# Kernel optimization log

Measured on AMD Instinct MI355X. Metric: run time of the kernel, lower is better.

Reference implementation:

```python
import jax, jax.numpy as jnp
import numpy as np

B, T, D = 2, 2048, 2048
H = 8
KEY_DIM, VAL_DIM = 1024, 2048   # expand_k=0.5, expand_v=1.0
HK, HV = KEY_DIM // H, VAL_DIM // H
LOW_RANK = 16
GATE_NORM = 16.0
CHUNK = 64
HIDDEN = (D * 4 * 2 // 3 + 63) // 64 * 64  # 5504, exactly as GLUFFN.__init__
EPS = 1e-6


def rmsnorm(x, w):
    return x * jax.lax.rsqrt(jnp.mean(x * x, axis=-1, keepdims=True) + EPS) * w


def setup_inputs() -> dict:
    key = jax.random.key(0)
    ks = jax.random.split(key, 12)
    w = lambda k, s: jax.random.normal(k, s, jnp.float32) * 0.02
    return {
        "x": jax.random.normal(ks[0], (B, T, D), jnp.float32),
        "norm1_w": jnp.ones((D,), jnp.float32),
        "wq": w(ks[1], (D, KEY_DIM)),
        "wk": w(ks[2], (D, KEY_DIM)),
        "wv": w(ks[3], (D, VAL_DIM)),
        "gk_w1": w(ks[4], (D, LOW_RANK)),
        "gk_w2": w(ks[5], (LOW_RANK, KEY_DIM)),
        "gk_b": jnp.zeros((KEY_DIM,), jnp.float32),
        "wg": w(ks[6], (D, VAL_DIM)),
        "gnorm_w": jnp.ones((HV,), jnp.float32),
        "wo": w(ks[7], (VAL_DIM, D)),
        "ffn_norm_w": jnp.ones((D,), jnp.float32),
        "w_gate": w(ks[8], (D, HIDDEN)),
        "w_up": w(ks[9], (D, HIDDEN)),
        "w_down": w(ks[10], (HIDDEN, D)),
    }


def _gla(h, wq, wk, wv, gk_w1, gk_w2, gk_b, wg, gnorm_w, wo):
    # Gated linear attention, chunk-parallel form (fla-style):
    #   S_t = diag(exp(g_t)) S_{t-1} + k_t^T v_t ;  o_t = q_t S_t
    Bb, Tt, _ = h.shape
    nc = Tt // CHUNK

    def split(t, hd):  # [B,T,H*hd] -> [nc,B,H,CHUNK,hd]
        t = t.reshape(Bb, nc, CHUNK, H, hd)
        return jnp.transpose(t, (1, 0, 3, 2, 4))

    q = split(h @ wq, HK) * (HK ** -0.5)
    k = split(h @ wk, HK)
    v = split(h @ wv, HV)
    # low-rank forget gate, log-sigmoid scaled by gate_logit_normalizer=16
    g = split(jax.nn.log_sigmoid(h @ gk_w1 @ gk_w2 + gk_b) / GATE_NORM, HK)

    mask = jnp.tril(jnp.ones((CHUNK, CHUNK), jnp.float32))

    def step(S, inp):
        qc, kc, vc, gc = inp                       # [B,H,C,*]
        b = jnp.cumsum(gc, axis=-2)                # cumulative log-decay within chunk
        qe = qc * jnp.exp(b)
        A = jnp.einsum('bhik,bhjk->bhij', qe, kc * jnp.exp(-b)) * mask
        o = jnp.einsum('bhck,bhkv->bhcv', qe, S) + jnp.einsum('bhij,bhjv->bhiv', A, vc)
        bl = b[:, :, -1:, :]                       # decay to end of chunk
        S = jnp.exp(bl[:, :, 0, :])[..., None] * S + \
            jnp.einsum('bhck,bhcv->bhkv', kc * jnp.exp(bl - b), vc)
        return S, o

    S0 = jnp.zeros((Bb, H, HK, HV), h.dtype)
    _, o = jax.lax.scan(step, S0, (q, k, v, g))    # o: [nc,B,H,C,HV]
    o = jnp.transpose(o, (1, 0, 3, 2, 4)).reshape(Bb, Tt, H, HV)

    gate = (h @ wg).reshape(Bb, Tt, H, HV)
    # per-head RMSNorm + swish output gate (FusedRMSNormSwishGate)
    o = rmsnorm(o, gnorm_w) * gate * jax.nn.sigmoid(gate)
    return o.reshape(Bb, Tt, VAL_DIM) @ wo


def reference(x, norm1_w, wq, wk, wv, gk_w1, gk_w2, gk_b, wg, gnorm_w, wo,
              ffn_norm_w, w_gate, w_up, w_down):
    h = rmsnorm(x, norm1_w)
    x = x + _gla(h, wq, wk, wv, gk_w1, gk_w2, gk_b, wg, gnorm_w, wo)
    h2 = rmsnorm(x, ffn_norm_w)
    ffn = (jax.nn.silu(h2 @ w_gate) * (h2 @ w_up)) @ w_down  # GLUFFN, dropout=eval
    return x + ffn
```

## Files before the change

kernel.cpp:

```cpp
#include <hip/hip_runtime.h>

typedef unsigned short u16;
typedef __attribute__((ext_vector_type(8))) short bh8;
typedef __attribute__((ext_vector_type(4))) float f4;

__device__ __forceinline__ float bf2f(u16 u) {
  union { unsigned int i; float f; } x; x.i = ((unsigned int)u) << 16; return x.f;
}
__device__ __forceinline__ u16 f2bf(float f) {
  union { float f; unsigned int i; } x; x.f = f;
  unsigned int r = x.i + 0x7fffu + ((x.i >> 16) & 1u);
  return (u16)(r >> 16);
}
__device__ __forceinline__ f4 mfma16(bh8 a, bh8 b, f4 c) {
  return __builtin_amdgcn_mfma_f32_16x16x32_bf16(a, b, c, 0, 0, 0);
}
__device__ __forceinline__ void gload16(const void* g, void* l) {
  __builtin_amdgcn_global_load_lds(
      (const __attribute__((address_space(1))) void*)g,
      (__attribute__((address_space(3))) void*)l, 16, 0, 0);
}
__device__ __forceinline__ void store_out(float* p, float v) { *p = v; }
__device__ __forceinline__ void store_out(u16* p, float v) { *p = f2bf(v); }

__device__ __forceinline__ bh8 rd8(const u16* arr, int row, int col, int rowbytes) {
  return *(const bh8*)((const char*)arr + row * rowbytes + ((col * 2) ^ ((row & 7) << 4)));
}

__global__ __launch_bounds__(256)
void wtrans_k(const float* __restrict__ src, u16* __restrict__ dst, int R, int C) {
  __shared__ float tile[32][33];
  int tx = threadIdx.x & 31, ty = threadIdx.x >> 5;
  int c0 = blockIdx.x * 32, r0 = blockIdx.y * 32;
#pragma unroll
  for (int yy = 0; yy < 32; yy += 8)
    tile[ty + yy][tx] = src[(size_t)(r0 + ty + yy) * C + c0 + tx];
  __syncthreads();
#pragma unroll
  for (int yy = 0; yy < 32; yy += 8)
    dst[(size_t)(c0 + ty + yy) * R + r0 + tx] = f2bf(tile[tx][ty + yy]);
}

__global__ __launch_bounds__(256)
void rmsnorm_k(const float* __restrict__ x, const float* __restrict__ w,
               u16* __restrict__ out) {
  int row = blockIdx.x, t = threadIdx.x;
  const float* xr = x + (size_t)row * 2048;
  float4 a = ((const float4*)xr)[t * 2];
  float4 b = ((const float4*)xr)[t * 2 + 1];
  float ss = a.x*a.x + a.y*a.y + a.z*a.z + a.w*a.w
           + b.x*b.x + b.y*b.y + b.z*b.z + b.w*b.w;
#pragma unroll
  for (int s = 32; s > 0; s >>= 1) ss += __shfl_xor(ss, s, 64);
  __shared__ float red[4];
  if ((t & 63) == 0) red[t >> 6] = ss;
  __syncthreads();
  float rr = rsqrtf((red[0] + red[1] + red[2] + red[3]) * (1.0f / 2048.0f) + 1e-6f);
  float v[8] = {a.x, a.y, a.z, a.w, b.x, b.y, b.z, b.w};
  int c0 = t * 8;
  u16* orow = out + (size_t)row * 2048 + c0;
#pragma unroll
  for (int j = 0; j < 8; ++j) orow[j] = f2bf(v[j] * rr * w[c0 + j]);
}

template <int EPI, typename OutT>
__global__ __launch_bounds__(256)
void gemm_bt(const u16* __restrict__ A, const u16* __restrict__ Bt,
             OutT* C, const void* aux, float scale, int M, int N, int K) {
  __shared__ u16 As[4096];
  __shared__ u16 Bs[4096];
  int t = threadIdx.x, lane = t & 63, wave = t >> 6;
  int m0 = blockIdx.y * 128, n0 = blockIdx.x * 128;
  int wr = (wave >> 1) * 64, wc = (wave & 1) * 64;
  int c_ = lane & 15, r_ = lane >> 4;
  f4 z4 = {0.f, 0.f, 0.f, 0.f};
  f4 acc[4][4];
#pragma unroll
  for (int m = 0; m < 4; ++m)
#pragma unroll
    for (int n = 0; n < 4; ++n) acc[m][n] = z4;

  const u16* Ab = A + (size_t)m0 * K;
  const u16* Bb = Bt + (size_t)n0 * K;
  int srow = t >> 2, scol = (t & 3) * 8;
  char* AsB = (char*)As;
  char* BsB = (char*)Bs;
  int ldsbase = wave * 1024;

  for (int k0 = 0; k0 < K; k0 += 32) {
#pragma unroll
    for (int p = 0; p < 2; ++p) {
      gload16(Ab + (size_t)(p * 64 + srow) * K + k0 + scol, AsB + p * 4096 + ldsbase);
      gload16(Bb + (size_t)(p * 64 + srow) * K + k0 + scol, BsB + p * 4096 + ldsbase);
    }
    __syncthreads();
    bh8 af[4], bfr[4];
#pragma unroll
    for (int m = 0; m < 4; ++m) af[m] = *(const bh8*)&As[(wr + m * 16 + c_) * 32 + r_ * 8];
#pragma unroll
    for (int n = 0; n < 4; ++n) bfr[n] = *(const bh8*)&Bs[(wc + n * 16 + c_) * 32 + r_ * 8];
#pragma unroll
    for (int m = 0; m < 4; ++m)
#pragma unroll
      for (int n = 0; n < 4; ++n) acc[m][n] = mfma16(af[m], bfr[n], acc[m][n]);
    __syncthreads();
  }
#pragma unroll
  for (int m = 0; m < 4; ++m) {
#pragma unroll
    for (int r = 0; r < 4; ++r) {
      int rowg = m0 + wr + m * 16 + r_ * 4 + r;
      size_t rb = (size_t)rowg * N;
#pragma unroll
      for (int n = 0; n < 4; ++n) {
        int colg = n0 + wc + n * 16 + c_;
        float val = acc[m][n][r];
        if (EPI == 0) {
          store_out(&C[rb + colg], val * scale);
        } else if (EPI == 1) {
          store_out(&C[rb + colg], val + ((const float*)aux)[rb + colg]);
        } else if (EPI == 2) {
          float gv = bf2f(((const u16*)aux)[rb + colg]);
          store_out(&C[rb + colg], val * (gv / (1.f + expf(-gv))));
        } else {
          int bb = rowg >> 11, t2 = rowg & 2047;
          int pan = ((bb << 5) + (t2 >> 6)) * 8 + (colg >> 8);
          int ii = t2 & 63, vv = colg & 255;
          *(u16*)((char*)C + (size_t)pan * 32768 + vv * 128 + ((ii * 2) ^ ((vv & 7) << 4)))
              = f2bf(val);
        }
      }
    }
  }
}

__global__ __launch_bounds__(256)
void lowrank_k(const u16* __restrict__ h, const float* __restrict__ w1,
               const float* __restrict__ w2, const float* __restrict__ bias,
               float* __restrict__ g) {
  int row = blockIdx.x, t = threadIdx.x, lane = t & 63, wave = t >> 6;
  const u16* hr = h + (size_t)row * 2048;
  bh8 hv = *(const bh8*)&hr[t * 8];
  float p[16];
#pragma unroll
  for (int j = 0; j < 16; ++j) p[j] = 0.f;
#pragma unroll
  for (int kk = 0; kk < 8; ++kk) {
    float f = bf2f((u16)hv[kk]);
    const float* wrow = w1 + (size_t)(t * 8 + kk) * 16;
#pragma unroll
    for (int j = 0; j < 16; ++j) p[j] += f * wrow[j];
  }
#pragma unroll
  for (int j = 0; j < 16; ++j)
#pragma unroll
    for (int s = 32; s > 0; s >>= 1) p[j] += __shfl_xor(p[j], s, 64);
  __shared__ float gl[4][16];
  if (lane == 0) {
#pragma unroll
    for (int j = 0; j < 16; ++j) gl[wave][j] = p[j];
  }
  __syncthreads();
  float glow[16];
#pragma unroll
  for (int j = 0; j < 16; ++j) glow[j] = gl[0][j] + gl[1][j] + gl[2][j] + gl[3][j];
  float* grow = g + (size_t)row * 1024;
#pragma unroll
  for (int nn = 0; nn < 4; ++nn) {
    int n = nn * 256 + t;
    float z = bias[n];
#pragma unroll
    for (int j = 0; j < 16; ++j) z += glow[j] * w2[j * 1024 + n];
    float ls = fminf(z, 0.f) - log1pf(expf(-fabsf(z)));
    grow[n] = ls * (1.0f / 16.0f);
  }
}

__global__ __launch_bounds__(128)
void gprep_k(u16* __restrict__ q, u16* __restrict__ k, const float* __restrict__ g,
             u16* __restrict__ keT, float* __restrict__ ebl) {
  int bid = blockIdx.x;
  int h = bid & 7, bc = bid >> 3;
  int b = bc >> 5, c = bc & 31;
  int ch = threadIdx.x;
  size_t base = ((size_t)(b * 2048 + c * 64)) * 1024 + h * 128 + ch;
  char* keTp = (char*)keT + (size_t)bid * 16384 + ch * 128;
  int sw = (ch & 7) << 4;
  float bacc = 0.f;
  for (int i8 = 0; i8 < 8; ++i8) {
    u16 kp[8];
#pragma unroll
    for (int e = 0; e < 8; ++e) {
      size_t off = base + (size_t)(i8 * 8 + e) * 1024;
      bacc += g[off];
      float eb = __expf(bacc);
      float reb = __builtin_amdgcn_rcpf(eb);
      float qv = bf2f(q[off]), kv = bf2f(k[off]);
      q[off] = f2bf(qv * eb);
      u16 kev = f2bf(kv * reb);
      k[off] = kev;
      kp[e] = kev;
    }
    *(bh8*)(keTp + ((i8 * 16) ^ sw)) = *(const bh8*)kp;
  }
  ebl[(size_t)bid * 128 + ch] = __expf(bacc);
}

__global__ __launch_bounds__(256)
void gla_scan(const u16* __restrict__ qg, const u16* __restrict__ kg,
              const u16* __restrict__ keTg, const u16* __restrict__ vTg,
              const float* __restrict__ eblg, float* __restrict__ outp) {
  __shared__ u16 qeL[64 * 128];
  __shared__ u16 keL[64 * 128];
  __shared__ u16 kTL[128 * 64];
  __shared__ u16 vTL[64 * 64];
  __shared__ u16 AL[64 * 64];
  __shared__ u16 SbL[64 * 128];
  __shared__ float SfL[64][133];

  int t = threadIdx.x, lane = t & 63, w = t >> 6;
  int vb = blockIdx.x & 3, bh = blockIdx.x >> 2;
  int b = bh >> 3, h = bh & 7;
  int c_ = lane & 15, r_ = lane >> 4;
  f4 z4 = {0.f, 0.f, 0.f, 0.f};

  for (int i = t; i < 64 * 128; i += 256) SbL[i] = 0;
  for (int i = t; i < 64 * 133; i += 256) ((float*)SfL)[i] = 0.f;

  const char* qbase = (const char*)qg + (size_t)b * 2048 * 2048 + h * 256;
  const char* kbase = (const char*)kg + (size_t)b * 2048 * 2048 + h * 256;
  int rowoff = (t >> 4) * 2048 + (t & 15) * 16;
  int4 pq[4], pk[4], pkt[4], pvt[2];

#define LOADCH(cc)                                                              \
  {                                                                             \
    const char* qc = qbase + (size_t)(cc) * 64 * 2048;                          \
    const char* kc = kbase + (size_t)(cc) * 64 * 2048;                          \
    int panel_ = ((b * 32 + (cc)) * 8 + h);                                     \
    const char* ktc = (const char*)keTg + (size_t)panel_ * 16384;               \
    const char* vtc = (const char*)vTg + (size_t)panel_ * 32768 + vb * 8192;    \
    _Pragma("unroll")                                                           \
    for (int j = 0; j < 4; ++j) {                                               \
      pq[j] = *(const int4*)(qc + j * 16 * 2048 + rowoff);                      \
      pk[j] = *(const int4*)(kc + j * 16 * 2048 + rowoff);                      \
      pkt[j] = *(const int4*)(ktc + j * 4096 + t * 16);                         \
    }                                                                           \
    _Pragma("unroll")                                                           \
    for (int j = 0; j < 2; ++j) pvt[j] = *(const int4*)(vtc + j * 4096 + t * 16); \
  }

  LOADCH(0);
  for (int c = 0; c < 32; ++c) {
#pragma unroll
    for (int j = 0; j < 4; ++j) {
      int L = j * 4096 + t * 16;
      int d = (L & ~255) | ((L & 255) ^ (((L >> 8) & 7) << 4));
      *(int4*)((char*)qeL + d) = pq[j];
      *(int4*)((char*)keL + d) = pk[j];
      *(int4*)((char*)kTL + L) = pkt[j];
    }
#pragma unroll
    for (int j = 0; j < 2; ++j) *(int4*)((char*)vTL + j * 4096 + t * 16) = pvt[j];
    if (c < 31) LOADCH(c + 1);
    int panel = ((b * 32 + c) * 8 + h);
    float eblr[2][4];
#pragma unroll
    for (int kt = 0; kt < 2; ++kt)
#pragma unroll
      for (int r = 0; r < 4; ++r)
        eblr[kt][r] = eblg[(size_t)panel * 128 + w * 32 + kt * 16 + r_ * 4 + r];
    __syncthreads();

    f4 accA[4] = {z4, z4, z4, z4};
    f4 accS[2][4] = {{z4, z4, z4, z4}, {z4, z4, z4, z4}};
#pragma unroll
    for (int ks = 0; ks < 4; ++ks) {
      bh8 a = rd8(qeL, w * 16 + c_, ks * 32 + r_ * 8, 256);
#pragma unroll
      for (int n = 0; n < 4; ++n)
        accA[n] = mfma16(a, rd8(keL, n * 16 + c_, ks * 32 + r_ * 8, 256), accA[n]);
    }
#pragma unroll
    for (int ks = 0; ks < 2; ++ks) {
      bh8 bf_[4];
#pragma unroll
      for (int n = 0; n < 4; ++n) bf_[n] = rd8(vTL, n * 16 + c_, ks * 32 + r_ * 8, 128);
#pragma unroll
      for (int kt = 0; kt < 2; ++kt) {
        bh8 a = rd8(kTL, w * 32 + kt * 16 + c_, ks * 32 + r_ * 8, 128);
#pragma unroll
        for (int n = 0; n < 4; ++n) accS[kt][n] = mfma16(a, bf_[n], accS[kt][n]);
      }
    }
#pragma unroll
    for (int n = 0; n < 4; ++n)
#pragma unroll
      for (int r = 0; r < 4; ++r) {
        int i = w * 16 + r_ * 4 + r, j = n * 16 + c_;
        *(u16*)((char*)AL + i * 128 + ((j * 2) ^ ((i & 7) << 4))) =
            (j <= i) ? f2bf(accA[n][r]) : (u16)0;
      }
    __syncthreads();

    f4 acco[4] = {z4, z4, z4, z4};
#pragma unroll
    for (int ks = 0; ks < 4; ++ks) {
      bh8 a = rd8(qeL, w * 16 + c_, ks * 32 + r_ * 8, 256);
#pragma unroll
      for (int n = 0; n < 4; ++n)
        acco[n] = mfma16(a, rd8(SbL, n * 16 + c_, ks * 32 + r_ * 8, 256), acco[n]);
    }
#pragma unroll
    for (int ks = 0; ks < 2; ++ks) {
      bh8 a = rd8(AL, w * 16 + c_, ks * 32 + r_ * 8, 128);
#pragma unroll
      for (int n = 0; n < 4; ++n)
        acco[n] = mfma16(a, rd8(vTL, n * 16 + c_, ks * 32 + r_ * 8, 128), acco[n]);
    }
    {
      size_t obase = (size_t)(b * 2048 + c * 64 + w * 16 + r_ * 4) * 2048 + h * 256 + vb * 64;
#pragma unroll
      for (int n = 0; n < 4; ++n)
#pragma unroll
        for (int r = 0; r < 4; ++r)
          outp[obase + (size_t)r * 2048 + n * 16 + c_] = acco[n][r];
    }
    __syncthreads();

#pragma unroll
    for (int kt = 0; kt < 2; ++kt)
#pragma unroll
      for (int n = 0; n < 4; ++n)
#pragma unroll
        for (int r = 0; r < 4; ++r) {
          int kk = w * 32 + kt * 16 + r_ * 4 + r;
          int vcol = n * 16 + c_;
          float nv = eblr[kt][r] * (SfL[vcol][kk] + accS[kt][n][r]);
          SfL[vcol][kk] = nv;
          *(u16*)((char*)SbL + vcol * 256 + ((kk * 2) ^ ((vcol & 7) << 4))) = f2bf(nv);
        }
    __syncthreads();
  }
#undef LOADCH
}

__global__ __launch_bounds__(256)
void ogate_k(const float* __restrict__ o, const u16* __restrict__ gate,
             const float* __restrict__ gw, u16* __restrict__ og) {
  int tok = blockIdx.x, t = threadIdx.x;
  int head = t >> 5, l32 = t & 31, v0 = l32 * 8;
  size_t base = (size_t)tok * 2048 + head * 256 + v0;
  float4 a = *(const float4*)&o[base];
  float4 b = *(const float4*)&o[base + 4];
  float ov[8] = {a.x, a.y, a.z, a.w, b.x, b.y, b.z, b.w};
  float ss = 0.f;
#pragma unroll
  for (int j = 0; j < 8; ++j) ss += ov[j] * ov[j];
#pragma unroll
  for (int s = 16; s > 0; s >>= 1) ss += __shfl_xor(ss, s, 32);
  float rr = rsqrtf(ss * (1.0f / 256.0f) + 1e-6f);
#pragma unroll
  for (int j = 0; j < 8; ++j) {
    float gv = bf2f(gate[base + j]);
    float val = ov[j] * rr * gw[v0 + j];
    og[base + j] = f2bf(val * gv / (1.f + expf(-gv)));
  }
}

extern "C" void kernel_launch(void* const* d_in, const int* in_sizes, int n_in,
                              void* d_out, int out_size, void* d_ws, size_t ws_size,
                              hipStream_t stream) {
  (void)in_sizes; (void)n_in; (void)out_size; (void)ws_size;
  const float* x = (const float*)d_in[0];
  const float* n1w = (const float*)d_in[1];
  const float* wq = (const float*)d_in[2];
  const float* wk = (const float*)d_in[3];
  const float* wv = (const float*)d_in[4];
  const float* gw1 = (const float*)d_in[5];
  const float* gw2 = (const float*)d_in[6];
  const float* gb = (const float*)d_in[7];
  const float* wg = (const float*)d_in[8];
  const float* gnw = (const float*)d_in[9];
  const float* wo = (const float*)d_in[10];
  const float* fnw = (const float*)d_in[11];
  const float* wgate = (const float*)d_in[12];
  const float* wup = (const float*)d_in[13];
  const float* wdown = (const float*)d_in[14];
  float* out = (float*)d_out;

  char* ws = (char*)d_ws;
  size_t off = 0;
  auto alloc = [&](size_t bytes) { size_t p = off; off += (bytes + 255) & ~(size_t)255; return p; };
  u16* wqT = (u16*)(ws + alloc(2ull * 1024 * 2048));
  u16* wkT = (u16*)(ws + alloc(2ull * 1024 * 2048));
  u16* wvT = (u16*)(ws + alloc(2ull * 2048 * 2048));
  u16* wgT = (u16*)(ws + alloc(2ull * 2048 * 2048));
  u16* woT = (u16*)(ws + alloc(2ull * 2048 * 2048));
  u16* wgateT = (u16*)(ws + alloc(2ull * 5504 * 2048));
  u16* wupT = (u16*)(ws + alloc(2ull * 5504 * 2048));
  u16* wdT = (u16*)(ws + alloc(2ull * 2048 * 5504));
  u16* h_bf = (u16*)(ws + alloc(2ull * 4096 * 2048));
  u16* q_bf = (u16*)(ws + alloc(2ull * 4096 * 1024));
  u16* k_bf = (u16*)(ws + alloc(2ull * 4096 * 1024));
  u16* vT_g = (u16*)(ws + alloc(2ull * 4096 * 2048));
  u16* gate_bf = (u16*)(ws + alloc(2ull * 4096 * 2048));
  float* g_f = (float*)(ws + alloc(4ull * 4096 * 1024));
  float* o_f = (float*)(ws + alloc(4ull * 4096 * 2048));
  u16* gH = (u16*)(ws + alloc(2ull * 4096 * 5504));
  float* ebl_g = (float*)(ws + alloc(4ull * 512 * 128));
  u16* keT_g = h_bf;
  u16* og = h_bf;
  u16* h2 = q_bf;
  float* x2 = o_f;
  u16* mid = gH;

  dim3 blk(256);
  wtrans_k<<<dim3(32, 64), blk, 0, stream>>>(wq, wqT, 2048, 1024);
  wtrans_k<<<dim3(32, 64), blk, 0, stream>>>(wk, wkT, 2048, 1024);
  wtrans_k<<<dim3(64, 64), blk, 0, stream>>>(wv, wvT, 2048, 2048);
  wtrans_k<<<dim3(64, 64), blk, 0, stream>>>(wg, wgT, 2048, 2048);
  wtrans_k<<<dim3(64, 64), blk, 0, stream>>>(wo, woT, 2048, 2048);
  wtrans_k<<<dim3(172, 64), blk, 0, stream>>>(wgate, wgateT, 2048, 5504);
  wtrans_k<<<dim3(172, 64), blk, 0, stream>>>(wup, wupT, 2048, 5504);
  wtrans_k<<<dim3(64, 172), blk, 0, stream>>>(wdown, wdT, 5504, 2048);

  rmsnorm_k<<<4096, blk, 0, stream>>>(x, n1w, h_bf);

  gemm_bt<0, u16><<<dim3(8, 32), blk, 0, stream>>>(h_bf, wqT, q_bf, nullptr, 0.08838834764831845f, 4096, 1024, 2048);
  gemm_bt<0, u16><<<dim3(8, 32), blk, 0, stream>>>(h_bf, wkT, k_bf, nullptr, 1.f, 4096, 1024, 2048);
  gemm_bt<3, u16><<<dim3(16, 32), blk, 0, stream>>>(h_bf, wvT, vT_g, nullptr, 1.f, 4096, 2048, 2048);
  gemm_bt<0, u16><<<dim3(16, 32), blk, 0, stream>>>(h_bf, wgT, gate_bf, nullptr, 1.f, 4096, 2048, 2048);
  lowrank_k<<<4096, blk, 0, stream>>>(h_bf, gw1, gw2, gb, g_f);

  gprep_k<<<512, dim3(128), 0, stream>>>(q_bf, k_bf, g_f, keT_g, ebl_g);

  gla_scan<<<64, blk, 0, stream>>>(q_bf, k_bf, keT_g, vT_g, ebl_g, o_f);

  ogate_k<<<4096, blk, 0, stream>>>(o_f, gate_bf, gnw, og);

  gemm_bt<1, float><<<dim3(16, 32), blk, 0, stream>>>(og, woT, x2, x, 1.f, 4096, 2048, 2048);

  rmsnorm_k<<<4096, blk, 0, stream>>>(x2, fnw, h2);

  gemm_bt<0, u16><<<dim3(43, 32), blk, 0, stream>>>(h2, wgateT, gH, nullptr, 1.f, 4096, 5504, 2048);
  gemm_bt<2, u16><<<dim3(43, 32), blk, 0, stream>>>(h2, wupT, mid, gH, 1.f, 4096, 5504, 2048);
  gemm_bt<1, float><<<dim3(16, 32), blk, 0, stream>>>(mid, wdT, out, x2, 1.f, 4096, 2048, 5504);
}
```

Baseline: 1.141 ms.

## Replace GEMM with triple-buffered 128x256 kernel and fuse projection GEMMs

Replaces the single-stage 128x128 GEMM with a 128x256-tile kernel. It triple-buffers LDS through direct global-to-LDS loads, uses an XOR-swizzled LDS layout, and splits each k-step into two MFMA phases separated by barriers, with s_setprio raised around the MFMAs. Block order is remapped in groups of eight to improve cache locality. The q/k and v/gate projections are each merged into one wider GEMM, relying on the transposed weights being adjacent in the workspace. The gate and up weights are row-interleaved so a single GEMM pairs each gate value with its up value through a lane shuffle and writes the SwiGLU result directly. This removes the separate gate-output round trip and several launches, but raises register and LDS pressure per block.

```diff
diff --git a/kernel.cpp b/kernel.cpp
--- a/kernel.cpp
+++ b/kernel.cpp
@@ -20,15 +20,14 @@
       (const __attribute__((address_space(1))) void*)g,
       (__attribute__((address_space(3))) void*)l, 16, 0, 0);
 }
-__device__ __forceinline__ void store_out(float* p, float v) { *p = v; }
-__device__ __forceinline__ void store_out(u16* p, float v) { *p = f2bf(v); }
 
 __device__ __forceinline__ bh8 rd8(const u16* arr, int row, int col, int rowbytes) {
   return *(const bh8*)((const char*)arr + row * rowbytes + ((col * 2) ^ ((row & 7) << 4)));
 }
 
 __global__ __launch_bounds__(256)
-void wtrans_k(const float* __restrict__ src, u16* __restrict__ dst, int R, int C) {
+void wtrans_k(const float* __restrict__ src, u16* __restrict__ dst, int R, int C,
+              int rmul, int roff) {
   __shared__ float tile[32][33];
   int tx = threadIdx.x & 31, ty = threadIdx.x >> 5;
   int c0 = blockIdx.x * 32, r0 = blockIdx.y * 32;
@@ -38,7 +37,7 @@
   __syncthreads();
 #pragma unroll
   for (int yy = 0; yy < 32; yy += 8)
-    dst[(size_t)(c0 + ty + yy) * R + r0 + tx] = f2bf(tile[tx][ty + yy]);
+    dst[(size_t)((c0 + ty + yy) * rmul + roff) * R + r0 + tx] = f2bf(tile[tx][ty + yy]);
 }
 
 __global__ __launch_bounds__(256)
@@ -64,70 +63,137 @@
 }
 
 template <int EPI, typename OutT>
-__global__ __launch_bounds__(256)
-void gemm_bt(const u16* __restrict__ A, const u16* __restrict__ Bt,
-             OutT* C, const void* aux, float scale, int M, int N, int K) {
-  __shared__ u16 As[4096];
-  __shared__ u16 Bs[4096];
-  int t = threadIdx.x, lane = t & 63, wave = t >> 6;
-  int m0 = blockIdx.y * 128, n0 = blockIdx.x * 128;
-  int wr = (wave >> 1) * 64, wc = (wave & 1) * 64;
+__global__ __launch_bounds__(256, 2)
+void gemm2(const u16* __restrict__ A, const u16* __restrict__ Bt,
+           OutT* __restrict__ C, void* __restrict__ aux, float scale,
+           int M, int N, int K, int gx) {
+  __shared__ char lds[73728];
+  int t = threadIdx.x, lane = t & 63, w = t >> 6;
   int c_ = lane & 15, r_ = lane >> 4;
+
+  int nwg = gridDim.x;
+  int wg = (blockIdx.x & 7) * (nwg >> 3) + (blockIdx.x >> 3);
+  int gy = nwg / gx;
+  int bx = wg / gy, by = wg % gy;
+  int m0 = by * 128, n0 = bx * 256;
+
+  const size_t ldA = K, ldB = K;
+
+  auto stageA = [&](int kt, int slot, int h) {
+    int p = h * 256 + t;
+    int cc = p ^ ((p >> 3) & 7);
+    int m = cc >> 2, kb = cc & 3;
+    const char* src = (const char*)A + ((size_t)(m0 + m) * ldA + kt * 32) * 2 + kb * 16;
+    char* dst = lds + slot * 24576 + h * 4096 + w * 1024;
+    gload16(src, dst);
+  };
+  auto stageB = [&](int kt, int slot, int qq, int j) {
+    int p = qq * 512 + j * 256 + t;
+    int cc = p ^ ((p >> 3) & 7);
+    int n = cc >> 2, kb = cc & 3;
+    const char* src = (const char*)Bt + ((size_t)(n0 + n) * ldB + kt * 32) * 2 + kb * 16;
+    char* dst = lds + slot * 24576 + 8192 + (qq * 8192 + j * 4096) + w * 1024;
+    gload16(src, dst);
+  };
+  auto rdA = [&](int slot, int mb) -> bh8 {
+    int cc = (mb * 16 + c_) * 4 + r_;
+    int p = cc ^ ((cc >> 3) & 7);
+    return *(const bh8*)(lds + slot * 24576 + p * 16);
+  };
+  auto rdB = [&](int slot, int nb) -> bh8 {
+    int cc = (w * 64 + nb * 16 + c_) * 4 + r_;
+    int p = cc ^ ((cc >> 3) & 7);
+    return *(const bh8*)(lds + slot * 24576 + 8192 + p * 16);
+  };
+
   f4 z4 = {0.f, 0.f, 0.f, 0.f};
-  f4 acc[4][4];
-#pragma unroll
-  for (int m = 0; m < 4; ++m)
-#pragma unroll
-    for (int n = 0; n < 4; ++n) acc[m][n] = z4;
-
-  const u16* Ab = A + (size_t)m0 * K;
-  const u16* Bb = Bt + (size_t)n0 * K;
-  int srow = t >> 2, scol = (t & 3) * 8;
-  char* AsB = (char*)As;
-  char* BsB = (char*)Bs;
-  int ldsbase = wave * 1024;
-
-  for (int k0 = 0; k0 < K; k0 += 32) {
-#pragma unroll
-    for (int p = 0; p < 2; ++p) {
-      gload16(Ab + (size_t)(p * 64 + srow) * K + k0 + scol, AsB + p * 4096 + ldsbase);
-      gload16(Bb + (size_t)(p * 64 + srow) * K + k0 + scol, BsB + p * 4096 + ldsbase);
-    }
-    __syncthreads();
-    bh8 af[4], bfr[4];
-#pragma unroll
-    for (int m = 0; m < 4; ++m) af[m] = *(const bh8*)&As[(wr + m * 16 + c_) * 32 + r_ * 8];
-#pragma unroll
-    for (int n = 0; n < 4; ++n) bfr[n] = *(const bh8*)&Bs[(wc + n * 16 + c_) * 32 + r_ * 8];
-#pragma unroll
-    for (int m = 0; m < 4; ++m)
-#pragma unroll
-      for (int n = 0; n < 4; ++n) acc[m][n] = mfma16(af[m], bfr[n], acc[m][n]);
-    __syncthreads();
-  }
-#pragma unroll
-  for (int m = 0; m < 4; ++m) {
-#pragma unroll
-    for (int r = 0; r < 4; ++r) {
-      int rowg = m0 + wr + m * 16 + r_ * 4 + r;
-      size_t rb = (size_t)rowg * N;
-#pragma unroll
-      for (int n = 0; n < 4; ++n) {
-        int colg = n0 + wc + n * 16 + c_;
-        float val = acc[m][n][r];
-        if (EPI == 0) {
-          store_out(&C[rb + colg], val * scale);
-        } else if (EPI == 1) {
-          store_out(&C[rb + colg], val + ((const float*)aux)[rb + colg]);
-        } else if (EPI == 2) {
-          float gv = bf2f(((const u16*)aux)[rb + colg]);
-          store_out(&C[rb + colg], val * (gv / (1.f + expf(-gv))));
-        } else {
-          int bb = rowg >> 11, t2 = rowg & 2047;
-          int pan = ((bb << 5) + (t2 >> 6)) * 8 + (colg >> 8);
-          int ii = t2 & 63, vv = colg & 255;
-          *(u16*)((char*)C + (size_t)pan * 32768 + vv * 128 + ((ii * 2) ^ ((vv & 7) << 4)))
-              = f2bf(val);
+  f4 acc[8][4];
+#pragma unroll
+  for (int mb = 0; mb < 8; ++mb)
+#pragma unroll
+    for (int nb = 0; nb < 4; ++nb) acc[mb][nb] = z4;
+
+  int NT = K >> 5;
+  stageA(0, 0, 0); stageB(0, 0, 0, 0); stageB(0, 0, 0, 1);
+  stageA(0, 0, 1); stageB(0, 0, 1, 0); stageB(0, 0, 1, 1);
+  stageA(1, 1, 0); stageB(1, 1, 0, 0); stageB(1, 1, 0, 1);
+  stageA(1, 1, 1); stageB(1, 1, 1, 0); stageB(1, 1, 1, 1);
+  asm volatile("s_waitcnt vmcnt(6)" ::: "memory");
+  __builtin_amdgcn_s_barrier();
+  asm volatile("" ::: "memory");
+
+  int slot = 0;
+  for (int kt = 0; kt < NT; ++kt) {
+    int fslot = slot + 2; if (fslot >= 3) fslot -= 3;
+    int kts = kt + 2; if (kts >= NT) kts -= NT;
+    bh8 bfr[4], afr[4];
+#pragma unroll
+    for (int nb = 0; nb < 4; ++nb) bfr[nb] = rdB(slot, nb);
+#pragma unroll
+    for (int mb = 0; mb < 4; ++mb) afr[mb] = rdA(slot, mb);
+    stageA(kts, fslot, 0); stageB(kts, fslot, 0, 0); stageB(kts, fslot, 0, 1);
+    __builtin_amdgcn_s_barrier();
+    asm volatile("s_waitcnt lgkmcnt(0)" ::: "memory");
+    __builtin_amdgcn_sched_barrier(0);
+    __builtin_amdgcn_s_setprio(1);
+#pragma unroll
+    for (int mb = 0; mb < 4; ++mb)
+#pragma unroll
+      for (int nb = 0; nb < 4; ++nb) acc[mb][nb] = mfma16(afr[mb], bfr[nb], acc[mb][nb]);
+    __builtin_amdgcn_s_setprio(0);
+    __builtin_amdgcn_sched_barrier(0);
+    __builtin_amdgcn_s_barrier();
+    asm volatile("" ::: "memory");
+#pragma unroll
+    for (int mb = 0; mb < 4; ++mb) afr[mb] = rdA(slot, mb + 4);
+    stageA(kts, fslot, 1); stageB(kts, fslot, 1, 0); stageB(kts, fslot, 1, 1);
+    asm volatile("s_waitcnt vmcnt(6)" ::: "memory");
+    __builtin_amdgcn_s_barrier();
+    asm volatile("s_waitcnt lgkmcnt(0)" ::: "memory");
+    __builtin_amdgcn_sched_barrier(0);
+    __builtin_amdgcn_s_setprio(1);
+#pragma unroll
+    for (int mb = 0; mb < 4; ++mb)
+#pragma unroll
+      for (int nb = 0; nb < 4; ++nb) acc[mb + 4][nb] = mfma16(afr[mb], bfr[nb], acc[mb + 4][nb]);
+    __builtin_amdgcn_s_setprio(0);
+    __builtin_amdgcn_sched_barrier(0);
+    __builtin_amdgcn_s_barrier();
+    asm volatile("" ::: "memory");
+    slot = (slot + 1 == 3) ? 0 : slot + 1;
+  }
+  asm volatile("s_waitcnt vmcnt(0)" ::: "memory");
+
+#pragma unroll
+  for (int mb = 0; mb < 8; ++mb) {
+#pragma unroll
+    for (int rr = 0; rr < 4; ++rr) {
+      int row = m0 + mb * 16 + r_ * 4 + rr;
+#pragma unroll
+      for (int nb = 0; nb < 4; ++nb) {
+        int col = n0 + w * 64 + nb * 16 + c_;
+        float val = acc[mb][nb][rr];
+        if (EPI == 1) {
+          ((float*)C)[(size_t)row * N + col] = val + ((const float*)aux)[(size_t)row * N + col];
+        } else if (EPI == 5) {
+          if (col < 1024) ((u16*)C)[(size_t)row * 1024 + col] = f2bf(val * scale);
+          else ((u16*)aux)[(size_t)row * 1024 + col - 1024] = f2bf(val);
+        } else if (EPI == 4) {
+          if (col < 2048) {
+            int bb = row >> 11, t2 = row & 2047;
+            int pan = ((bb << 5) + (t2 >> 6)) * 8 + (col >> 8);
+            int ii = t2 & 63, vv = col & 255;
+            *(u16*)((char*)C + (size_t)pan * 32768 + vv * 128 + ((ii * 2) ^ ((vv & 7) << 4)))
+                = f2bf(val);
+          } else {
+            ((u16*)aux)[(size_t)row * 2048 + col - 2048] = f2bf(val);
+          }
+        } else if (EPI == 6) {
+          float other = __shfl_xor(val, 1, 64);
+          if (lane & 1) {
+            float gv = other;
+            ((u16*)C)[(size_t)row * 5504 + (col >> 1)] = f2bf(val * (gv / (1.f + expf(-gv))));
+          }
         }
       }
     }
@@ -396,8 +462,7 @@
   u16* wvT = (u16*)(ws + alloc(2ull * 2048 * 2048));
   u16* wgT = (u16*)(ws + alloc(2ull * 2048 * 2048));
   u16* woT = (u16*)(ws + alloc(2ull * 2048 * 2048));
-  u16* wgateT = (u16*)(ws + alloc(2ull * 5504 * 2048));
-  u16* wupT = (u16*)(ws + alloc(2ull * 5504 * 2048));
+  u16* btGU = (u16*)(ws + alloc(2ull * 11008 * 2048));
   u16* wdT = (u16*)(ws + alloc(2ull * 2048 * 5504));
   u16* h_bf = (u16*)(ws + alloc(2ull * 4096 * 2048));
   u16* q_bf = (u16*)(ws + alloc(2ull * 4096 * 1024));
@@ -406,30 +471,29 @@
   u16* gate_bf = (u16*)(ws + alloc(2ull * 4096 * 2048));
   float* g_f = (float*)(ws + alloc(4ull * 4096 * 1024));
   float* o_f = (float*)(ws + alloc(4ull * 4096 * 2048));
-  u16* gH = (u16*)(ws + alloc(2ull * 4096 * 5504));
+  u16* mid = (u16*)(ws + alloc(2ull * 4096 * 5504));
   float* ebl_g = (float*)(ws + alloc(4ull * 512 * 128));
   u16* keT_g = h_bf;
   u16* og = h_bf;
   u16* h2 = q_bf;
   float* x2 = o_f;
-  u16* mid = gH;
 
   dim3 blk(256);
-  wtrans_k<<<dim3(32, 64), blk, 0, stream>>>(wq, wqT, 2048, 1024);
-  wtrans_k<<<dim3(32, 64), blk, 0, stream>>>(wk, wkT, 2048, 1024);
-  wtrans_k<<<dim3(64, 64), blk, 0, stream>>>(wv, wvT, 2048, 2048);
-  wtrans_k<<<dim3(64, 64), blk, 0, stream>>>(wg, wgT, 2048, 2048);
-  wtrans_k<<<dim3(64, 64), blk, 0, stream>>>(wo, woT, 2048, 2048);
-  wtrans_k<<<dim3(172, 64), blk, 0, stream>>>(wgate, wgateT, 2048, 5504);
-  wtrans_k<<<dim3(172, 64), blk, 0, stream>>>(wup, wupT, 2048, 5504);
-  wtrans_k<<<dim3(64, 172), blk, 0, stream>>>(wdown, wdT, 5504, 2048);
+  wtrans_k<<<dim3(32, 64), blk, 0, stream>>>(wq, wqT, 2048, 1024, 1, 0);
+  wtrans_k<<<dim3(32, 64), blk, 0, stream>>>(wk, wkT, 2048, 1024, 1, 0);
+  wtrans_k<<<dim3(64, 64), blk, 0, stream>>>(wv, wvT, 2048, 2048, 1, 0);
+  wtrans_k<<<dim3(64, 64), blk, 0, stream>>>(wg, wgT, 2048, 2048, 1, 0);
+  wtrans_k<<<dim3(64, 64), blk, 0, stream>>>(wo, woT, 2048, 2048, 1, 0);
+  wtrans_k<<<dim3(172, 64), blk, 0, stream>>>(wgate, btGU, 2048, 5504, 2, 0);
+  wtrans_k<<<dim3(172, 64), blk, 0, stream>>>(wup, btGU, 2048, 5504, 2, 1);
+  wtrans_k<<<dim3(64, 172), blk, 0, stream>>>(wdown, wdT, 5504, 2048, 1, 0);
 
   rmsnorm_k<<<4096, blk, 0, stream>>>(x, n1w, h_bf);
 
-  gemm_bt<0, u16><<<dim3(8, 32), blk, 0, stream>>>(h_bf, wqT, q_bf, nullptr, 0.08838834764831845f, 4096, 1024, 2048);
-  gemm_bt<0, u16><<<dim3(8, 32), blk, 0, stream>>>(h_bf, wkT, k_bf, nullptr, 1.f, 4096, 1024, 2048);
-  gemm_bt<3, u16><<<dim3(16, 32), blk, 0, stream>>>(h_bf, wvT, vT_g, nullptr, 1.f, 4096, 2048, 2048);
-  gemm_bt<0, u16><<<dim3(16, 32), blk, 0, stream>>>(h_bf, wgT, gate_bf, nullptr, 1.f, 4096, 2048, 2048);
+  gemm2<5, u16><<<256, blk, 0, stream>>>(h_bf, wqT, q_bf, k_bf, 0.08838834764831845f,
+                                         4096, 2048, 2048, 8);
+  gemm2<4, u16><<<512, blk, 0, stream>>>(h_bf, wvT, vT_g, gate_bf, 1.f,
+                                         4096, 4096, 2048, 16);
   lowrank_k<<<4096, blk, 0, stream>>>(h_bf, gw1, gw2, gb, g_f);
 
   gprep_k<<<512, dim3(128), 0, stream>>>(q_bf, k_bf, g_f, keT_g, ebl_g);
@@ -438,11 +502,13 @@
 
   ogate_k<<<4096, blk, 0, stream>>>(o_f, gate_bf, gnw, og);
 
-  gemm_bt<1, float><<<dim3(16, 32), blk, 0, stream>>>(og, woT, x2, x, 1.f, 4096, 2048, 2048);
+  gemm2<1, float><<<256, blk, 0, stream>>>(og, woT, x2, (void*)x, 1.f,
+                                           4096, 2048, 2048, 8);
 
   rmsnorm_k<<<4096, blk, 0, stream>>>(x2, fnw, h2);
 
-  gemm_bt<0, u16><<<dim3(43, 32), blk, 0, stream>>>(h2, wgateT, gH, nullptr, 1.f, 4096, 5504, 2048);
-  gemm_bt<2, u16><<<dim3(43, 32), blk, 0, stream>>>(h2, wupT, mid, gH, 1.f, 4096, 5504, 2048);
-  gemm_bt<1, float><<<dim3(16, 32), blk, 0, stream>>>(mid, wdT, out, x2, 1.f, 4096, 2048, 5504);
-}
+  gemm2<6, u16><<<1376, blk, 0, stream>>>(h2, btGU, mid, nullptr, 1.f,
+                                          4096, 11008, 2048, 43);
+  gemm2<1, float><<<256, blk, 0, stream>>>(mid, wdT, out, x2, 1.f,
+                                           4096, 2048, 5504, 8);
+}
```

Result: faster. 1.081 ms (-5.3%).
